# Kernel tuning notes

Measured on AMD Instinct MI355X. Metric: run time of the kernel, lower is better.

## Reference

```python
import jax, jax.numpy as jnp
import numpy as np

N_NODES = 50000
N_EDGES = 500000
IN_CH = 128
HID = 64
HEADS = 4
N_LAYERS = 3
OUT_CH = 16
N_GRAPHS = 64
NEG_SLOPE = 0.2  # PyG GATConv default


def setup_inputs() -> dict:
    key = jax.random.key(0)
    ks = jax.random.split(key, 20)
    inp = {
        'x': jax.random.normal(ks[0], (N_NODES, IN_CH), dtype=jnp.float32),
        'edge_attr': jax.random.normal(ks[1], (N_EDGES, 8), dtype=jnp.float32),
        'edge_index': jax.random.randint(ks[2], (2, N_EDGES), 0, N_NODES, dtype=jnp.int64),
        'batch': jnp.sort(jax.random.randint(ks[3], (N_NODES,), 0, N_GRAPHS, dtype=jnp.int64)),
    }
    kidx = 4
    in_dim = IN_CH
    for i in range(N_LAYERS):
        inp[f'W{i}'] = jax.random.normal(ks[kidx], (in_dim, HEADS * HID), dtype=jnp.float32) * (1.0 / np.sqrt(in_dim)); kidx += 1
        inp[f'asrc{i}'] = jax.random.normal(ks[kidx], (HEADS, HID), dtype=jnp.float32) * 0.1; kidx += 1
        inp[f'adst{i}'] = jax.random.normal(ks[kidx], (HEADS, HID), dtype=jnp.float32) * 0.1; kidx += 1
        inp[f'b{i}'] = jnp.zeros((HEADS * HID,), dtype=jnp.float32)
        in_dim = HEADS * HID
    inp['Wc'] = jax.random.normal(ks[kidx], (HEADS * HID, OUT_CH), dtype=jnp.float32) * (1.0 / np.sqrt(HEADS * HID)); kidx += 1
    inp['bc'] = jnp.zeros((OUT_CH,), dtype=jnp.float32)
    return inp


def _gat_layer(x, src, dst, W, asrc, adst, b):
    # x: [N, F_in] -> h: [N, H, C]
    N = x.shape[0]
    h = (x @ W).reshape(N, HEADS, HID)
    s_src = jnp.einsum('nhc,hc->nh', h, asrc)  # [N, H]
    s_dst = jnp.einsum('nhc,hc->nh', h, adst)
    e = jax.nn.leaky_relu(s_src[src] + s_dst[dst], NEG_SLOPE)  # [E, H]
    # segment softmax over incoming edges of each destination node
    m = jax.ops.segment_max(e, dst, num_segments=N)            # [N, H]
    ex = jnp.exp(e - m[dst])
    denom = jax.ops.segment_sum(ex, dst, num_segments=N)       # [N, H]
    alpha = ex / (denom[dst] + 1e-16)                           # [E, H]
    out = jax.ops.segment_sum(alpha[:, :, None] * h[src], dst, num_segments=N)  # [N, H, C]
    return out.reshape(N, HEADS * HID) + b


def reference(x, edge_attr, edge_index, batch,
              W0, asrc0, adst0, b0,
              W1, asrc1, adst1, b1,
              W2, asrc2, adst2, b2,
              Wc, bc):
    N = x.shape[0]
    loop = jnp.arange(N, dtype=edge_index.dtype)
    # PyG GATConv adds self-loops by default
    src = jnp.concatenate([edge_index[0], loop])
    dst = jnp.concatenate([edge_index[1], loop])
    params = [(W0, asrc0, adst0, b0), (W1, asrc1, adst1, b1), (W2, asrc2, adst2, b2)]
    h = x
    for (W, asrc, adst, b) in params:
        h = jax.nn.relu(_gat_layer(h, src, dst, W, asrc, adst, b))
        # nn.Dropout(0.5) is identity in eval mode
    pooled = jax.ops.segment_sum(h, batch, num_segments=N_GRAPHS)  # global_add_pool
    return pooled @ Wc + bc
```

## Files before the change

kernel.cpp:

```cpp
#include <hip/hip_runtime.h>
#include <hip/hip_bf16.h>

#define NNODES 50000
#define NEDGES 500000
#define INCH 128
#define HID 64
#define HEADS 4
#define FDIM 256
#define NGRAPHS 64
#define OUTCH 16
#define NEG_SLOPE 0.2f

#define BM 64
#define BN 256
#define BK 32

typedef float f32x4 __attribute__((ext_vector_type(4)));
typedef _Float16 f16x8 __attribute__((ext_vector_type(8)));
typedef _Float16 f16x4 __attribute__((ext_vector_type(4)));

__device__ inline void gld_lds16(const void* g, void* l) {
    __builtin_amdgcn_global_load_lds((__attribute__((address_space(1))) void*)g,
                                     (__attribute__((address_space(3))) void*)l, 16, 0, 0);
}


__global__ void k_hist(const int* __restrict__ dst, int E, int* __restrict__ counts) {
    int i = blockIdx.x * blockDim.x + threadIdx.x;
    if (i < E) atomicAdd(&counts[dst[i]], 1);
}

__global__ __launch_bounds__(256) void k_blocksum(const int* __restrict__ counts, int N,
                                                  int* __restrict__ bsum) {
    int idx = blockIdx.x * 256 + threadIdx.x;
    int v = (idx < N) ? counts[idx] : 0;
#pragma unroll
    for (int off = 32; off; off >>= 1) v += __shfl_xor(v, off);
    __shared__ int wsum[4];
    if ((threadIdx.x & 63) == 0) wsum[threadIdx.x >> 6] = v;
    __syncthreads();
    if (threadIdx.x == 0) bsum[blockIdx.x] = wsum[0] + wsum[1] + wsum[2] + wsum[3];
}

__global__ __launch_bounds__(256) void k_scanfinal(const int* __restrict__ counts,
                                                   const int* __restrict__ bsum, int N,
                                                   int* __restrict__ rowstart,
                                                   int* __restrict__ cursor) {
    __shared__ int tmp[256];
    __shared__ int wsum[4];
    int t = threadIdx.x, b = blockIdx.x;
    int p = 0;
    for (int i = t; i < b; i += 256) p += bsum[i];
#pragma unroll
    for (int off = 32; off; off >>= 1) p += __shfl_xor(p, off);
    int idx = b * 256 + t;
    int v = (idx < N) ? counts[idx] : 0;
    tmp[t] = v;
    if ((t & 63) == 0) wsum[t >> 6] = p;
    __syncthreads();
    int bp = wsum[0] + wsum[1] + wsum[2] + wsum[3];
    for (int off = 1; off < 256; off <<= 1) {
        int u = (t >= off) ? tmp[t - off] : 0;
        __syncthreads();
        tmp[t] += u;
        __syncthreads();
    }
    if (idx < N) {
        int incl = bp + tmp[t];
        rowstart[idx + 1] = incl;
        cursor[idx] = incl - v;
    }
    if (idx == 0) rowstart[0] = 0;
}

__global__ void k_scatter(const int* __restrict__ src, const int* __restrict__ dst, int E,
                          int* __restrict__ cursor, int* __restrict__ csr_src) {
    int i = blockIdx.x * blockDim.x + threadIdx.x;
    if (i < E) {
        int p = atomicAdd(&cursor[dst[i]], 1);
        csr_src[p] = src[i];
    }
}


__global__ void k_wdecomp(const float* __restrict__ W, _Float16* __restrict__ Wt, int K) {
    int i = blockIdx.x * 256 + threadIdx.x;
    if (i >= K * 256) return;
    int k = i >> 8, n = i & 255;
    Wt[n * K + k] = (_Float16)W[i];
}


__global__ void k_adecomp(const float* __restrict__ X, _Float16* __restrict__ Xf, int total4) {
    int i = blockIdx.x * 256 + threadIdx.x;
    if (i >= total4) return;
    float4 v = ((const float4*)X)[i];
    f16x4 o = {(_Float16)v.x, (_Float16)v.y, (_Float16)v.z, (_Float16)v.w};
    ((f16x4*)Xf)[i] = o;
}


__global__ __launch_bounds__(256) void k_gemm_mfma(
    const _Float16* __restrict__ A, const _Float16* __restrict__ B,
    const float* __restrict__ av, const float* __restrict__ dv,
    _Float16* __restrict__ Hf,
    float* __restrict__ ssrcO, float* __restrict__ sdstO, int M, int K) {
    __shared__ _Float16 sA[2][BM * BK];
    __shared__ _Float16 sB[2][BN * BK];

    const int t = threadIdx.x;
    const int row0 = blockIdx.x * BM;
    const int wv = t >> 6, ln = t & 63, lr = ln & 15, lk = ln >> 4;

    const int ar = wv * 16 + (ln >> 2);
    const int alc = (ln & 3) ^ ((ar >> 1) & 3);
    const size_t agoff = (size_t)min(row0 + ar, M - 1) * K + alc * 8;
    const int brr = wv * 16 + (ln >> 2);
    const int fsc = lk ^ ((lr >> 1) & 3);

    f32x4 acc[4][4] = {};
    const int nt = K / BK;

#define STAGE(tt, p)                                                        \
    do {                                                                    \
        int _k0 = (tt)*BK;                                                  \
        gld_lds16(A + agoff + _k0, &sA[p][wv * 512]);                       \
        _Pragma("unroll") for (int _j = 0; _j < 4; ++_j) {                  \
            int _br = _j * 64 + brr;                                        \
            int _blc = (ln & 3) ^ ((_br >> 1) & 3);                         \
            gld_lds16(B + (size_t)_br * K + _k0 + _blc * 8,                 \
                      &sB[p][_j * 2048 + wv * 512]);                        \
        }                                                                   \
    } while (0)

    STAGE(0, 0);
    __syncthreads();
    for (int tt = 0; tt < nt; ++tt) {
        int cur = tt & 1;
        if (tt + 1 < nt) STAGE(tt + 1, cur ^ 1);

        f16x8 af[4];
#pragma unroll
        for (int mi = 0; mi < 4; ++mi)
            af[mi] = *(const f16x8*)&sA[cur][(mi * 16 + lr) * BK + fsc * 8];
#pragma unroll
        for (int ni = 0; ni < 4; ++ni) {
            f16x8 bf = *(const f16x8*)&sB[cur][(wv * 64 + ni * 16 + lr) * BK + fsc * 8];
#pragma unroll
            for (int mi = 0; mi < 4; ++mi)
                acc[mi][ni] = __builtin_amdgcn_mfma_f32_16x16x32_f16(af[mi], bf, acc[mi][ni], 0, 0, 0);
        }
        __syncthreads();
    }
#undef STAGE

    float ps[4][4] = {}, pd[4][4] = {};
#pragma unroll
    for (int ni = 0; ni < 4; ++ni) {
        int col = wv * 64 + ni * 16 + lr;
        float a_s = av[col], a_d = dv[col];
#pragma unroll
        for (int mi = 0; mi < 4; ++mi) {
            f32x4 v = acc[mi][ni];
            int r = row0 + mi * 16 + lk * 4;
#pragma unroll
            for (int j = 0; j < 4; ++j) {
                if (r + j < M) Hf[(size_t)(r + j) * FDIM + col] = (_Float16)v[j];
                ps[mi][j] += v[j] * a_s;
                pd[mi][j] += v[j] * a_d;
            }
        }
    }
#pragma unroll
    for (int mi = 0; mi < 4; ++mi) {
#pragma unroll
        for (int j = 0; j < 4; ++j) {
            float s = ps[mi][j], q = pd[mi][j];
            s += __shfl_xor(s, 1); s += __shfl_xor(s, 2);
            s += __shfl_xor(s, 4); s += __shfl_xor(s, 8);
            q += __shfl_xor(q, 1); q += __shfl_xor(q, 2);
            q += __shfl_xor(q, 4); q += __shfl_xor(q, 8);
            if (lr == 0) {
                int r = row0 + mi * 16 + lk * 4 + j;
                if (r < M) {
                    ssrcO[r * HEADS + wv] = s;
                    sdstO[r * HEADS + wv] = q;
                }
            }
        }
    }
}


__global__ __launch_bounds__(256) void k_aggregate(
    const _Float16* __restrict__ hf,
    const float* __restrict__ ssrc, const float* __restrict__ sdst,
    const int* __restrict__ rowstart, const int* __restrict__ csr_src,
    const float* __restrict__ bias,
    _Float16* __restrict__ outf, int N) {
    int wv = threadIdx.x >> 6, ln = threadIdx.x & 63;
    int n = blockIdx.x * 4 + wv;
    if (n >= N) return;
    int head = ln >> 4;
    int fo = head * 64 + (ln & 15) * 4;
    float sd = sdst[n * HEADS + head];
    float e = ssrc[n * HEADS + head] + sd;
    e = (e > 0.f) ? e : NEG_SLOPE * e;
    float m = e, d = 1.0f;
    f16x4 sv = *(const f16x4*)&hf[(size_t)n * FDIM + fo];
    float4 acc = make_float4((float)sv[0], (float)sv[1], (float)sv[2], (float)sv[3]);
    int r0 = rowstart[n], r1 = rowstart[n + 1];
    int cnt = r1 - r0;
    for (int base = 0; base < cnt; base += 8) {
        int s[8];
        f16x4 u[8];
        float c[8], w[8];
#pragma unroll
        for (int i = 0; i < 8; ++i) s[i] = csr_src[min(r0 + base + i, r1 - 1)];
#pragma unroll
        for (int i = 0; i < 8; ++i) u[i] = *(const f16x4*)&hf[(size_t)s[i] * FDIM + fo];
#pragma unroll
        for (int i = 0; i < 8; ++i) {
            float sc = ssrc[s[i] * HEADS + head] + sd;
            sc = (sc > 0.f) ? sc : NEG_SLOPE * sc;
            c[i] = (base + i < cnt) ? sc : -1e30f;
        }
        float mx = fmaxf(fmaxf(fmaxf(c[0], c[1]), fmaxf(c[2], c[3])),
                         fmaxf(fmaxf(c[4], c[5]), fmaxf(c[6], c[7])));
        float mn = fmaxf(m, mx);
        float wa = __expf(m - mn);
#pragma unroll
        for (int i = 0; i < 8; ++i) w[i] = __expf(c[i] - mn);
        float sx = 0.f, sy = 0.f, sz = 0.f, sw = 0.f, sdn = 0.f;
#pragma unroll
        for (int i = 0; i < 8; ++i) {
            sx += w[i] * (float)u[i][0];
            sy += w[i] * (float)u[i][1];
            sz += w[i] * (float)u[i][2];
            sw += w[i] * (float)u[i][3];
            sdn += w[i];
        }
        acc.x = acc.x * wa + sx;
        acc.y = acc.y * wa + sy;
        acc.z = acc.z * wa + sz;
        acc.w = acc.w * wa + sw;
        d = d * wa + sdn;
        m = mn;
    }
    float inv = 1.0f / d;
    float4 bv = *(const float4*)&bias[fo];
    f16x4 o;
    o[0] = (_Float16)fmaxf(acc.x * inv + bv.x, 0.f);
    o[1] = (_Float16)fmaxf(acc.y * inv + bv.y, 0.f);
    o[2] = (_Float16)fmaxf(acc.z * inv + bv.z, 0.f);
    o[3] = (_Float16)fmaxf(acc.w * inv + bv.w, 0.f);
    *(f16x4*)&outf[(size_t)n * FDIM + fo] = o;
}


__global__ __launch_bounds__(256) void k_pool(const _Float16* __restrict__ hf,
                                              const int* __restrict__ batch,
                                              float* __restrict__ pooled, int N) {
    int f = threadIdx.x;
    int n0 = blockIdx.x * 128;
    if (n0 >= N) return;
    int n1 = min(n0 + 128, N);
    int g = batch[n0];
    float run = 0.f;
    for (int n = n0; n < n1; ++n) {
        int gn = batch[n];
        if (gn != g) {
            atomicAdd(&pooled[g * FDIM + f], run);
            run = 0.f;
            g = gn;
        }
        run += (float)hf[(size_t)n * FDIM + f];
    }
    atomicAdd(&pooled[g * FDIM + f], run);
}


__global__ __launch_bounds__(256) void k_final(const float* __restrict__ pooled,
                                               const float* __restrict__ Wc,
                                               const float* __restrict__ bc,
                                               float* __restrict__ out) {
    int tid = blockIdx.x * 256 + threadIdx.x;
    int g = tid >> 4, o = tid & 15;
    float s = bc[o];
    for (int k = 0; k < FDIM; ++k) s += pooled[g * FDIM + k] * Wc[k * OUTCH + o];
    out[g * OUTCH + o] = s;
}


extern "C" void kernel_launch(void* const* d_in, const int* in_sizes, int n_in,
                              void* d_out, int out_size, void* d_ws, size_t ws_size,
                              hipStream_t stream) {
    const float* x = (const float*)d_in[0];
    const int* edge_index = (const int*)d_in[2];
    const int* batch = (const int*)d_in[3];
    const float* W[3]    = {(const float*)d_in[4], (const float*)d_in[8],  (const float*)d_in[12]};
    const float* asrc[3] = {(const float*)d_in[5], (const float*)d_in[9],  (const float*)d_in[13]};
    const float* adst[3] = {(const float*)d_in[6], (const float*)d_in[10], (const float*)d_in[14]};
    const float* bias[3] = {(const float*)d_in[7], (const float*)d_in[11], (const float*)d_in[15]};
    const float* Wc = (const float*)d_in[16];
    const float* bc = (const float*)d_in[17];

    const int N = in_sizes[3];
    const int E = in_sizes[2] / 2;
    const int* e_src = edge_index;
    const int* e_dst = edge_index + E;

    char* ws = (char*)d_ws;
    size_t off = 0;
    _Float16* hb = (_Float16*)(ws + off); off += (size_t)N * FDIM * 2;
    _Float16* xf = (_Float16*)(ws + off); off += (size_t)N * INCH * 2;
    _Float16* P  = (_Float16*)(ws + off); off += (size_t)N * FDIM * 2;
    float* ssrc = (float*)(ws + off); off += (size_t)N * HEADS * 4;
    float* sdst = (float*)(ws + off); off += (size_t)N * HEADS * 4;
    int* rowstart = (int*)(ws + off); off += ((size_t)(N + 1) * 4 + 255) / 256 * 256;
    int* counts = (int*)(ws + off); off += (size_t)N * 4;
    int* cursor = (int*)(ws + off); off += (size_t)N * 4;
    int* csr_src = (int*)(ws + off); off += (size_t)E * 4;
    float* pooled = (float*)(ws + off); off += (size_t)NGRAPHS * FDIM * 4;
    int* bsum = (int*)(ws + off); off += ((size_t)((N + 255) / 256) * 4 + 255) / 256 * 256;
    _Float16* Wt[3];
    int Ks[3] = {INCH, FDIM, FDIM};
    for (int l = 0; l < 3; ++l) {
        Wt[l] = (_Float16*)(ws + off); off += (size_t)256 * Ks[l] * 2;
    }

    const int nb = (N + 255) / 256;

    hipMemsetAsync(counts, 0, (size_t)N * 4, stream);
    k_hist<<<(E + 255) / 256, 256, 0, stream>>>(e_dst, E, counts);
    k_blocksum<<<nb, 256, 0, stream>>>(counts, N, bsum);
    k_scanfinal<<<nb, 256, 0, stream>>>(counts, bsum, N, rowstart, cursor);
    k_scatter<<<(E + 255) / 256, 256, 0, stream>>>(e_src, e_dst, E, cursor, csr_src);

    k_adecomp<<<((N * INCH / 4) + 255) / 256, 256, 0, stream>>>(x, xf, N * INCH / 4);
    for (int l = 0; l < 3; ++l)
        k_wdecomp<<<(Ks[l] * 256 + 255) / 256, 256, 0, stream>>>(W[l], Wt[l], Ks[l]);

    const _Float16* Af = xf;
    for (int l = 0; l < 3; ++l) {
        int K = Ks[l];
        k_gemm_mfma<<<(N + BM - 1) / BM, 256, 0, stream>>>(Af, Wt[l], asrc[l], adst[l],
                                                           hb, ssrc, sdst, N, K);
        k_aggregate<<<(N + 3) / 4, 256, 0, stream>>>(hb, ssrc, sdst, rowstart, csr_src,
                                                     bias[l], P, N);
        Af = P;
    }

    hipMemsetAsync(pooled, 0, (size_t)NGRAPHS * FDIM * 4, stream);
    k_pool<<<(N + 127) / 128, 256, 0, stream>>>(P, batch, pooled, N);
    k_final<<<4, 256, 0, stream>>>(pooled, Wc, bc, (float*)d_out);
}
```

Measured before the change: 341.3 us.

## Merge conversion kernels, simplify GEMM B staging, widen aggregate edge batch

Combines the input and three weight fp16 conversion kernels into a single launch to reduce launch overhead. Reuses the A-tile row/swizzle indices for the B-tile global-to-LDS staging, dropping redundant index math. Doubles the aggregation edge batch from 8 to 16 so more gather loads are in flight per iteration, at the cost of more registers and more wasted lanes for low-degree nodes. The merged kernel drops bounds checks and relies on sizes dividing exactly.

```diff
diff --git a/kernel.cpp b/kernel.cpp
--- a/kernel.cpp
+++ b/kernel.cpp
@@ -83,20 +83,31 @@
 }
 
 
-__global__ void k_wdecomp(const float* __restrict__ W, _Float16* __restrict__ Wt, int K) {
-    int i = blockIdx.x * 256 + threadIdx.x;
-    if (i >= K * 256) return;
+__device__ inline void wdecomp_body(const float* __restrict__ W, _Float16* __restrict__ Wt,
+                                    int K, int bb) {
+    int i = bb * 256 + threadIdx.x;
     int k = i >> 8, n = i & 255;
     Wt[n * K + k] = (_Float16)W[i];
 }
 
-
-__global__ void k_adecomp(const float* __restrict__ X, _Float16* __restrict__ Xf, int total4) {
-    int i = blockIdx.x * 256 + threadIdx.x;
-    if (i >= total4) return;
-    float4 v = ((const float4*)X)[i];
-    f16x4 o = {(_Float16)v.x, (_Float16)v.y, (_Float16)v.z, (_Float16)v.w};
-    ((f16x4*)Xf)[i] = o;
+__global__ __launch_bounds__(256) void k_convert(
+    const float* __restrict__ X, _Float16* __restrict__ Xf, int bx,
+    const float* __restrict__ W0, _Float16* __restrict__ Wt0,
+    const float* __restrict__ W1, _Float16* __restrict__ Wt1,
+    const float* __restrict__ W2, _Float16* __restrict__ Wt2) {
+    int b = blockIdx.x;
+    if (b < bx) {
+        int i = b * 256 + threadIdx.x;
+        float4 v = ((const float4*)X)[i];
+        f16x4 o = {(_Float16)v.x, (_Float16)v.y, (_Float16)v.z, (_Float16)v.w};
+        ((f16x4*)Xf)[i] = o;
+    } else if (b < bx + 128) {
+        wdecomp_body(W0, Wt0, INCH, b - bx);
+    } else if (b < bx + 384) {
+        wdecomp_body(W1, Wt1, FDIM, b - bx - 128);
+    } else {
+        wdecomp_body(W2, Wt2, FDIM, b - bx - 384);
+    }
 }
 
 
@@ -115,7 +126,6 @@
     const int ar = wv * 16 + (ln >> 2);
     const int alc = (ln & 3) ^ ((ar >> 1) & 3);
     const size_t agoff = (size_t)min(row0 + ar, M - 1) * K + alc * 8;
-    const int brr = wv * 16 + (ln >> 2);
     const int fsc = lk ^ ((lr >> 1) & 3);
 
     f32x4 acc[4][4] = {};
@@ -126,9 +136,8 @@
         int _k0 = (tt)*BK;                                                  \
         gld_lds16(A + agoff + _k0, &sA[p][wv * 512]);                       \
         _Pragma("unroll") for (int _j = 0; _j < 4; ++_j) {                  \
-            int _br = _j * 64 + brr;                                        \
-            int _blc = (ln & 3) ^ ((_br >> 1) & 3);                         \
-            gld_lds16(B + (size_t)_br * K + _k0 + _blc * 8,                 \
+            int _br = _j * 64 + ar;                                         \
+            gld_lds16(B + (size_t)_br * K + _k0 + alc * 8,                  \
                       &sB[p][_j * 2048 + wv * 512]);                        \
         }                                                                   \
     } while (0)
@@ -211,29 +220,30 @@
     float4 acc = make_float4((float)sv[0], (float)sv[1], (float)sv[2], (float)sv[3]);
     int r0 = rowstart[n], r1 = rowstart[n + 1];
     int cnt = r1 - r0;
-    for (int base = 0; base < cnt; base += 8) {
-        int s[8];
-        f16x4 u[8];
-        float c[8], w[8];
-#pragma unroll
-        for (int i = 0; i < 8; ++i) s[i] = csr_src[min(r0 + base + i, r1 - 1)];
-#pragma unroll
-        for (int i = 0; i < 8; ++i) u[i] = *(const f16x4*)&hf[(size_t)s[i] * FDIM + fo];
-#pragma unroll
-        for (int i = 0; i < 8; ++i) {
+    for (int base = 0; base < cnt; base += 16) {
+        int s[16];
+        f16x4 u[16];
+        float c[16], w[16];
+#pragma unroll
+        for (int i = 0; i < 16; ++i) s[i] = csr_src[min(r0 + base + i, r1 - 1)];
+#pragma unroll
+        for (int i = 0; i < 16; ++i) u[i] = *(const f16x4*)&hf[(size_t)s[i] * FDIM + fo];
+#pragma unroll
+        for (int i = 0; i < 16; ++i) {
             float sc = ssrc[s[i] * HEADS + head] + sd;
             sc = (sc > 0.f) ? sc : NEG_SLOPE * sc;
             c[i] = (base + i < cnt) ? sc : -1e30f;
         }
-        float mx = fmaxf(fmaxf(fmaxf(c[0], c[1]), fmaxf(c[2], c[3])),
-                         fmaxf(fmaxf(c[4], c[5]), fmaxf(c[6], c[7])));
+        float mx = c[0];
+#pragma unroll
+        for (int i = 1; i < 16; ++i) mx = fmaxf(mx, c[i]);
         float mn = fmaxf(m, mx);
         float wa = __expf(m - mn);
 #pragma unroll
-        for (int i = 0; i < 8; ++i) w[i] = __expf(c[i] - mn);
+        for (int i = 0; i < 16; ++i) w[i] = __expf(c[i] - mn);
         float sx = 0.f, sy = 0.f, sz = 0.f, sw = 0.f, sdn = 0.f;
 #pragma unroll
-        for (int i = 0; i < 8; ++i) {
+        for (int i = 0; i < 16; ++i) {
             sx += w[i] * (float)u[i][0];
             sy += w[i] * (float)u[i][1];
             sz += w[i] * (float)u[i][2];
@@ -337,9 +347,11 @@
     k_scanfinal<<<nb, 256, 0, stream>>>(counts, bsum, N, rowstart, cursor);
     k_scatter<<<(E + 255) / 256, 256, 0, stream>>>(e_src, e_dst, E, cursor, csr_src);
 
-    k_adecomp<<<((N * INCH / 4) + 255) / 256, 256, 0, stream>>>(x, xf, N * INCH / 4);
-    for (int l = 0; l < 3; ++l)
-        k_wdecomp<<<(Ks[l] * 256 + 255) / 256, 256, 0, stream>>>(W[l], Wt[l], Ks[l]);
+    {
+        int bx = (N * INCH / 4) / 256;
+        int btot = bx + (Ks[0] * 256) / 256 + (Ks[1] * 256) / 256 + (Ks[2] * 256) / 256;
+        k_convert<<<btot, 256, 0, stream>>>(x, xf, bx, W[0], Wt[0], W[1], Wt[1], W[2], Wt[2]);
+    }
 
     const _Float16* Af = xf;
     for (int l = 0; l < 3; ++l) {
```

Result: slower. 384.3 us (+12.6%).
